# Performance work log

Hardware: AMD Instinct MI355X
Metric: run time of the kernel (lower is better)

Reference implementation:

```python
import jax, jax.numpy as jnp
import numpy as np

N, C, K, B, G = 32768, 128, 16, 4, 8
SCALE, BASE = 2.0, 10000.0

def _bn(x, gamma, beta, eps=1e-5):
    # torch BatchNorm1d (training): stats over all axes except channel (last)
    axes = tuple(range(x.ndim - 1))
    mean = x.mean(axes)
    var = x.var(axes)
    return (x - mean) / jnp.sqrt(var + eps) * gamma + beta

def _cayley_rope(x, coord, S_param):
    c = x.shape[-1]
    S = jnp.triu(S_param, 1)
    S = S - S.T
    I = jnp.eye(c, dtype=x.dtype)
    P = jnp.linalg.solve(I + S, I - S)  # (I+S)^-1 (I-S)
    xr = x @ P.T
    dpa = c // 3 // 2 * 2          # dim per axis (even)
    dr = dpa * 3                   # rotated dims
    inv_freq = 1.0 / (BASE ** (jnp.arange(0, dpa, 2, dtype=jnp.float32) / dpa))
    cs = coord * SCALE
    def rot(f, c1):
        ang = c1[:, None] * inv_freq[None, :]
        s, co = jnp.sin(ang), jnp.cos(ang)
        fr, fi = jnp.split(f, 2, axis=-1)
        return jnp.concatenate([fr * co - fi * s, fr * s + fi * co], -1)
    parts = [rot(xr[:, i * dpa:(i + 1) * dpa], cs[:, i]) for i in range(3)]
    out = jnp.concatenate(parts + [xr[:, dr:]], -1)
    return out @ P

def setup_inputs() -> dict:
    key = jax.random.key(0)
    ks = jax.random.split(key, 24)
    w = lambda k, i, o, s=0.02: jax.random.normal(k, (i, o), jnp.float32) * s
    inp = {
        'feat': jax.random.normal(ks[0], (N, C), jnp.float32),
        'coord': jax.random.uniform(ks[1], (N, 3), jnp.float32) * 10.0,
        'reference_index': jax.random.randint(ks[2], (N, K), 0, N),
        'offset': jnp.arange(1, B + 1, dtype=jnp.int32) * (N // B),
        'Wq': w(ks[3], C, C), 'bq': jnp.zeros((C,)),
        'gq': jnp.ones((C,)), 'bnq': jnp.zeros((C,)),
        'Wk': w(ks[4], C, C), 'bk': jnp.zeros((C,)),
        'gk': jnp.ones((C,)), 'bnk': jnp.zeros((C,)),
        'Wv': w(ks[5], C, C), 'bv': jnp.zeros((C,)),
        'S_param': jax.random.normal(ks[6], (C, C), jnp.float32) * 0.01,
        'Ww1': w(ks[7], C, G), 'bw1': jnp.zeros((G,)),
        'gw': jnp.ones((G,)), 'bnw': jnp.zeros((G,)),
        'Ww2': w(ks[8], G, G), 'bw2': jnp.zeros((G,)),
        'Wg1': w(ks[9], 2 * C, C), 'bg1': jnp.zeros((C,)),
        'gg': jnp.ones((C,)), 'bng': jnp.zeros((C,)),
        'Wg2': w(ks[10], C, G, 0.001), 'bg2': jnp.full((G,), 3.0),
    }
    return inp

def reference(feat, coord, reference_index, offset, Wq, bq, gq, bnq, Wk, bk, gk, bnk,
              Wv, bv, S_param, Ww1, bw1, gw, bnw, Ww2, bw2, Wg1, bg1, gg, bng, Wg2, bg2):
    q_raw = jax.nn.relu(_bn(feat @ Wq + bq, gq, bnq))
    k_raw = jax.nn.relu(_bn(feat @ Wk + bk, gk, bnk))
    value = feat @ Wv + bv
    q = _cayley_rope(q_raw, coord, S_param)
    k = _cayley_rope(k_raw, coord, S_param)
    kg = k[reference_index]            # [N,K,C] gather
    vg = value[reference_index]        # [N,K,C]
    rel = kg - q[:, None, :]
    geom = jax.nn.relu(_bn(rel @ Ww1 + bw1, gw, bnw)) @ Ww2 + bw2  # [N,K,G]
    seg = jnp.searchsorted(offset, jnp.arange(N), side='right')
    gmax = jax.ops.segment_max(q_raw, seg, num_segments=B)
    gate_in = jnp.concatenate([q_raw, gmax[seg]], -1)              # [N,2C]
    gate = jax.nn.sigmoid(jax.nn.relu(_bn(gate_in @ Wg1 + bg1, gg, bng)) @ Wg2 + bg2)  # [N,G]
    refined = geom * (1.0 + gate[:, None, :])
    attn = jax.nn.softmax(refined, axis=1)
    mask = jnp.sign(reference_index + 1).astype(attn.dtype)
    attn = attn * mask[:, :, None]
    vg4 = vg.reshape(N, K, G, C // G)
    out = jnp.einsum('nkgi,nkg->ngi', vg4, attn).reshape(N, C)
    return out
```

## Files before the change

### kernel.cpp

```cpp
#include <hip/hip_runtime.h>
#include <math.h>

#define N_PTS 32768
#define C_DIM 128
#define K_NB  16
#define G_DIM 8

#define OF_PW     0
#define OF_STATQ  1024
#define OF_STATK  1280
#define OF_STATG1 1536
#define OF_STATH  1792
#define OF_UMAXP  1808
#define OF_UMAXN  2320
#define OF_GSG    2832
#define OF_WQT    4096
#define OF_WKT    12288
#define OF_WVT    20480
#define OF_WG1T   28672
#define OF_PTMIT  36864
#define OF_QW     65536
#define OF_KW     327680
#define OF_GATE   589824
#define OF_G1     1048576
#define OF_V      5242880

typedef short bf16x8 __attribute__((ext_vector_type(8)));
typedef float f32x4  __attribute__((ext_vector_type(4)));

#define LSTR 136

__device__ __forceinline__ unsigned f2bf(float f) {
  unsigned u = __float_as_uint(f);
  return (u + 0x7fffu + ((u >> 16) & 1u)) >> 16;
}
__device__ __forceinline__ float bf2f(short s) {
  return __uint_as_float(((unsigned)(unsigned short)s) << 16);
}
__device__ __forceinline__ unsigned fenc(float f) {
  unsigned b = __float_as_uint(f);
  return (b & 0x80000000u) ? ~b : (b | 0x80000000u);
}
__device__ __forceinline__ float fdec(unsigned u) {
  unsigned b = (u & 0x80000000u) ? (u & 0x7fffffffu) : ~u;
  return __uint_as_float(b);
}
__device__ __forceinline__ bf16x8 pack_bf8(float4 a, float4 b) {
  bf16x8 r;
  r[0] = (short)f2bf(a.x); r[1] = (short)f2bf(a.y);
  r[2] = (short)f2bf(a.z); r[3] = (short)f2bf(a.w);
  r[4] = (short)f2bf(b.x); r[5] = (short)f2bf(b.y);
  r[6] = (short)f2bf(b.z); r[7] = (short)f2bf(b.w);
  return r;
}

__device__ __forceinline__ void g2l16(const void* g, void* l) {
  __builtin_amdgcn_global_load_lds(
      (const __attribute__((address_space(1))) void*)g,
      (__attribute__((address_space(3))) void*)l, 16, 0, 0);
}

__device__ __forceinline__ void stage_async(short* dst, const short* __restrict__ src, int tid) {
  int lane = tid & 63, wv = tid >> 6;
  #pragma unroll
  for (int it = 0; it < 8; ++it) {
    int chunk = it*256 + wv*64;
    int D = (chunk + lane)*16;
    int gs = D ^ (((D >> 8) & 7) << 4);
    g2l16((const char*)src + gs, (char*)dst + chunk*16);
  }
}

__device__ __forceinline__ f32x4 mfma1(const short* Bb, const bf16x8* a4, int row, int quad) {
  f32x4 ac = {0.f, 0.f, 0.f, 0.f};
  int sx = (row & 7) << 4;
  #pragma unroll
  for (int ks = 0; ks < 4; ++ks) {
    const char* p = (const char*)Bb + (((row*256) + ks*64 + quad*16) ^ sx);
    ac = __builtin_amdgcn_mfma_f32_16x16x32_bf16(a4[ks], *(const bf16x8*)p, ac, 0, 0, 0);
  }
  return ac;
}

__global__ __launch_bounds__(256) void cayley(const float* __restrict__ Sp,
    const float* __restrict__ Ww1,
    const float* __restrict__ Wq, const float* __restrict__ Wk,
    const float* __restrict__ Wv, const float* __restrict__ Wg1,
    short* __restrict__ WqT, short* __restrict__ WkT,
    short* __restrict__ WvT, short* __restrict__ Wg1T,
    short* __restrict__ PTmIT, float* __restrict__ PW,
    float* __restrict__ statz)
{
  __shared__ __align__(16) short Ssh[128*LSTR];
  __shared__ float x0[128], x1[128];
  int bx = blockIdx.x, tid = threadIdx.x;
  if (bx >= 64) {
    if (bx < 80) {
      int idx = bx - 64, widx = idx >> 2, qr = idx & 3;
      const float* src = (widx == 0) ? Wq : (widx == 1) ? Wk : (widx == 2) ? Wv : Wg1;
      short* dst = (widx == 0) ? WqT : (widx == 1) ? WkT : (widx == 2) ? WvT : Wg1T;
      const float4* s4 = (const float4*)src;
      short* T = Ssh;
      #pragma unroll
      for (int it = 0; it < 4; ++it) {
        int q = it*256 + tid; int kloc = q >> 5, n4 = q & 31;
        float4 v = s4[(qr*32 + kloc)*32 + n4];
        T[(n4*4+0)*40 + kloc] = (short)f2bf(v.x);
        T[(n4*4+1)*40 + kloc] = (short)f2bf(v.y);
        T[(n4*4+2)*40 + kloc] = (short)f2bf(v.z);
        T[(n4*4+3)*40 + kloc] = (short)f2bf(v.w);
      }
      __syncthreads();
      #pragma unroll
      for (int it = 0; it < 2; ++it) {
        int i2 = it*256 + tid;
        int n = i2 >> 2, part = i2 & 3;
        uint4 val = *(const uint4*)&T[n*40 + part*8];
        *(uint4*)&dst[n*128 + qr*32 + part*8] = val;
      }
    } else {
      #pragma unroll
      for (int it = 0; it < 8; ++it) {
        int idx = it*256 + tid;
        if (idx < 1808) statz[idx] = 0.f;
      }
    }
    return;
  }
  int c0 = bx*2, c1 = c0 + 1;
  {
    const float4* s4 = (const float4*)Sp;
    #pragma unroll
    for (int it = 0; it < 16; ++it) {
      int idx = it*256 + tid;
      int i = idx >> 5, j0 = (idx & 31) * 4;
      float4 v = s4[idx];
      #pragma unroll
      for (int u = 0; u < 4; ++u) {
        int j = j0 + u;
        float val = (&v.x)[u];
        if (j > i) {
          unsigned b = f2bf(val);
          Ssh[i*LSTR + j] = (short)b;
          Ssh[j*LSTR + i] = (short)(b ^ 0x8000u);
        } else if (j == i) {
          Ssh[i*LSTR + j] = 0;
        }
      }
    }
  }
  if (tid < 128) {
    x0[tid] = (tid == c0) ? 1.f : 0.f;
    x1[tid] = (tid == c1) ? 1.f : 0.f;
  }
  __syncthreads();
  int i = tid >> 1, h = tid & 1;
  const short* srow = &Ssh[i*LSTR + h*64];
  for (int t = 0; t < 16; ++t) {
    float a0 = 0.f, a1 = 0.f;
    #pragma unroll
    for (int jq = 0; jq < 16; ++jq) {
      short4 sv = *(const short4*)&srow[jq*4];
      #pragma unroll
      for (int u = 0; u < 4; ++u) {
        float s = bf2f((&sv.x)[u]);
        int j = h*64 + jq*4 + u;
        a0 = fmaf(s, x0[j], a0);
        a1 = fmaf(s, x1[j], a1);
      }
    }
    a0 += __shfl_xor(a0, 1);
    a1 += __shfl_xor(a1, 1);
    __syncthreads();
    if (h == 0) {
      x0[i] = a0 + ((i == c0) ? 1.f : 0.f);
      x1[i] = a1 + ((i == c1) ? 1.f : 0.f);
    }
    __syncthreads();
  }
  if (tid < 128) {
    PTmIT[c0*128 + tid] = (short)f2bf(2.f*x0[tid] - ((tid == c0) ? 2.f : 0.f));
  } else {
    int t = tid - 128;
    PTmIT[c1*128 + t] = (short)f2bf(2.f*x1[t] - ((t == c1) ? 2.f : 0.f));
  }
  if (tid < 16) {
    int cc = tid >> 3, g = tid & 7;
    const float* xv = cc ? x1 : x0;
    int c = cc ? c1 : c0;
    float acc = 0.f;
    #pragma unroll 8
    for (int j = 0; j < 128; ++j) acc = fmaf(xv[j], Ww1[j*8 + g], acc);
    PW[c*8 + g] = 2.f*acc - Ww1[c*8 + g];
  }
}

__global__ __launch_bounds__(256, 2) void qkv_mfma(const float* __restrict__ feat,
    const short* __restrict__ WqT, const short* __restrict__ WkT, const short* __restrict__ WvT,
    const float* __restrict__ bq, const float* __restrict__ bk, const float* __restrict__ bv,
    float* __restrict__ Vv,
    float* __restrict__ statq, float* __restrict__ statk,
    unsigned* __restrict__ umaxp, unsigned* __restrict__ umaxn)
{
  __shared__ __align__(16) short Bb0[128*128];
  __shared__ __align__(16) short Bb1[128*128];
  __shared__ float ssum[2][128], ssq[2][128];
  __shared__ unsigned ump[128], umn[128];
  int tid = threadIdx.x, row0 = blockIdx.x * 64, seg = row0 >> 13;
  int lane = tid & 63, w = tid >> 6, l15 = lane & 15, quad = lane >> 4;
  stage_async(Bb0, WqT, tid);
  if (tid < 128) {
    ssum[0][tid] = 0.f; ssum[1][tid] = 0.f;
    ssq[0][tid] = 0.f;  ssq[1][tid] = 0.f;
    ump[tid] = 0u; umn[tid] = 0u;
  }
  bf16x8 af[4];
  {
    long rbase = (long)(row0 + w*16 + l15) * 128;
    #pragma unroll
    for (int ks = 0; ks < 4; ++ks) {
      int c0 = ks*32 + quad*8;
      float4 v0 = *(const float4*)&feat[rbase + c0];
      float4 v1 = *(const float4*)&feat[rbase + c0 + 4];
      af[ks] = pack_bf8(v0, v1);
    }
  }
  __syncthreads();
  stage_async(Bb1, WkT, tid);
  {
    #pragma unroll
    for (int nt = 0; nt < 8; ++nt) {
      f32x4 ac = mfma1(Bb0, af, nt*16 + l15, quad);
      int col = nt*16 + l15;
      float bb = bq[col];
      float s = 0.f, s2 = 0.f, mx = -1e30f, mn = 1e30f;
      #pragma unroll
      for (int r = 0; r < 4; ++r) {
        float raw = ac[r];
        float v = raw + bb;
        s += v; s2 = fmaf(v, v, s2);
        mx = fmaxf(mx, raw); mn = fminf(mn, raw);
      }
      s += __shfl_xor(s, 16); s += __shfl_xor(s, 32);
      s2 += __shfl_xor(s2, 16); s2 += __shfl_xor(s2, 32);
      mx = fmaxf(mx, __shfl_xor(mx, 16)); mx = fmaxf(mx, __shfl_xor(mx, 32));
      mn = fminf(mn, __shfl_xor(mn, 16)); mn = fminf(mn, __shfl_xor(mn, 32));
      if (lane < 16) {
        atomicAdd(&ssum[0][col], s); atomicAdd(&ssq[0][col], s2);
        atomicMax(&ump[col], fenc(mx)); atomicMax(&umn[col], fenc(-mn));
      }
    }
  }
  __syncthreads();
  stage_async(Bb0, WvT, tid);
  {
    #pragma unroll
    for (int nt = 0; nt < 8; ++nt) {
      f32x4 ac = mfma1(Bb1, af, nt*16 + l15, quad);
      int col = nt*16 + l15;
      float bb = bk[col];
      float s = 0.f, s2 = 0.f;
      #pragma unroll
      for (int r = 0; r < 4; ++r) {
        float v = ac[r] + bb;
        s += v; s2 = fmaf(v, v, s2);
      }
      s += __shfl_xor(s, 16); s += __shfl_xor(s, 32);
      s2 += __shfl_xor(s2, 16); s2 += __shfl_xor(s2, 32);
      if (lane < 16) { atomicAdd(&ssum[1][col], s); atomicAdd(&ssq[1][col], s2); }
    }
  }
  __syncthreads();
  {
    #pragma unroll
    for (int nt = 0; nt < 8; ++nt) {
      f32x4 ac = mfma1(Bb0, af, nt*16 + l15, quad);
      int col = nt*16 + l15;
      float bb = bv[col];
      #pragma unroll
      for (int r = 0; r < 4; ++r)
        Vv[(long)(row0 + w*16 + quad*4 + r)*128 + col] = ac[r] + bb;
    }
  }
  __syncthreads();
  if (tid < 128) {
    atomicAdd(&statq[tid], ssum[0][tid]); atomicAdd(&statq[128 + tid], ssq[0][tid]);
    atomicAdd(&statk[tid], ssum[1][tid]); atomicAdd(&statk[128 + tid], ssq[1][tid]);
    atomicMax(&umaxp[seg*128 + tid], ump[tid]);
    atomicMax(&umaxn[seg*128 + tid], umn[tid]);
  }
}

__global__ __launch_bounds__(128) void gprep(
    const float* __restrict__ statq,
    const float* __restrict__ gq, const float* __restrict__ bnq,
    const float* __restrict__ bq,
    const unsigned* __restrict__ umaxp, const unsigned* __restrict__ umaxn,
    const float* __restrict__ Wg1, const float* __restrict__ bg1,
    float* __restrict__ gsgO)
{
  __shared__ float gml[128];
  int s = blockIdx.x, tid = threadIdx.x;
  const float invn = 1.f / 32768.f;
  {
    float m = statq[tid]*invn, vv = fmaf(-m, m, statq[128 + tid]*invn);
    float a = rsqrtf(vv + 1e-5f) * gq[tid];
    float b = fmaf(-m, a, bnq[tid]);
    float cb2 = fmaf(a, bq[tid], b);
    float mx = fdec(umaxp[s*128 + tid]);
    float mn = -fdec(umaxn[s*128 + tid]);
    gml[tid] = fmaxf(0.f, fmaxf(fmaf(a, mx, cb2), fmaf(a, mn, cb2)));
  }
  __syncthreads();
  float acc = bg1[tid];
  #pragma unroll 8
  for (int j = 0; j < 128; ++j)
    acc = fmaf(gml[j], Wg1[(128 + j)*128 + tid], acc);
  gsgO[s*128 + tid] = acc;
}

__global__ __launch_bounds__(256, 2) void rqkw(
    const float* __restrict__ feat,
    const short* __restrict__ WqT, const short* __restrict__ WkT,
    const short* __restrict__ PTmIT, const short* __restrict__ Wg1T,
    const float* __restrict__ coord,
    const float* __restrict__ bq, const float* __restrict__ bk,
    const float* __restrict__ statq, const float* __restrict__ statk,
    const float* __restrict__ gq, const float* __restrict__ bnq,
    const float* __restrict__ gk, const float* __restrict__ bnk,
    const float* __restrict__ gsgG,
    const float* __restrict__ PW, const float* __restrict__ bw1,
    float* __restrict__ qw, float* __restrict__ kw,
    float* __restrict__ g1, float* __restrict__ statg1)
{
  __shared__ __align__(16) char arena[81920];
  short* Bb0  = (short*)arena;
  short* Bb1  = (short*)(arena + 32768);
  char*  bnS  = arena + 65536;
  float* xsq  = (float*)arena;
  float* xsk  = (float*)(arena + 33792);
  float* pws  = (float*)(arena + 67584);
  float* ssum4 = (float*)(arena + 71680);
  float* ssq4  = (float*)(arena + 73728);
  int tid = threadIdx.x, row0 = blockIdx.x * 64, seg = row0 >> 13;
  int lane = tid & 63, w = tid >> 6, l15 = lane & 15, quad = lane >> 4;
  stage_async(Bb0, WqT, tid);
  stage_async(Bb1, WkT, tid);
  bf16x8 af[4];
  {
    long rbase = (long)(row0 + w*16 + l15) * 128;
    #pragma unroll
    for (int ks = 0; ks < 4; ++ks) {
      int c0 = ks*32 + quad*8;
      float4 v0 = *(const float4*)&feat[rbase + c0];
      float4 v1 = *(const float4*)&feat[rbase + c0 + 4];
      af[ks] = pack_bf8(v0, v1);
    }
  }
  float caRq[8], cbRq[8], caRk[8], cbRk[8];
  {
    const float invn = 1.f / 32768.f;
    #pragma unroll
    for (int nt = 0; nt < 8; ++nt) {
      int col = nt*16 + l15;
      float m = statq[col]*invn, vv = fmaf(-m, m, statq[128 + col]*invn);
      float a = rsqrtf(vv + 1e-5f) * gq[col];
      float b = fmaf(-m, a, bnq[col]);
      caRq[nt] = a; cbRq[nt] = fmaf(a, bq[col], b);
      m = statk[col]*invn; vv = fmaf(-m, m, statk[128 + col]*invn);
      a = rsqrtf(vv + 1e-5f) * gk[col];
      b = fmaf(-m, a, bnk[col]);
      caRk[nt] = a; cbRk[nt] = fmaf(a, bk[col], b);
    }
  }
  float gsR[8];
  #pragma unroll
  for (int nt = 0; nt < 8; ++nt)
    gsR[nt] = gsgG[seg*128 + nt*16 + l15];
  __syncthreads();
  float bnl_q[32], bnl_k[32];
  {
    #pragma unroll
    for (int nt = 0; nt < 8; ++nt) {
      f32x4 ac = mfma1(Bb0, af, nt*16 + l15, quad);
      int col = nt*16 + l15;
      float A = caRq[nt], B = cbRq[nt];
      #pragma unroll
      for (int r = 0; r < 4; ++r) {
        float v = fmaxf(0.f, fmaf(A, ac[r], B));
        bnl_q[nt*4 + r] = v;
        int row = w*16 + quad*4 + r;
        int ba = (row*256 + col*2) ^ ((row & 7) << 4);
        *(short*)(bnS + ba) = (short)f2bf(v);
      }
    }
  }
  __syncthreads();
  stage_async(Bb0, PTmIT, tid);
  {
    #pragma unroll
    for (int nt = 0; nt < 8; ++nt) {
      f32x4 ac = mfma1(Bb1, af, nt*16 + l15, quad);
      float A = caRk[nt], B = cbRk[nt];
      #pragma unroll
      for (int r = 0; r < 4; ++r)
        bnl_k[nt*4 + r] = fmaxf(0.f, fmaf(A, ac[r], B));
    }
  }
  __syncthreads();
  stage_async(Bb1, Wg1T, tid);
  bf16x8 af2q[4];
  {
    int rowA = w*16 + l15, sx2 = (rowA & 7) << 4;
    #pragma unroll
    for (int ks = 0; ks < 4; ++ks)
      af2q[ks] = *(const bf16x8*)(bnS + ((rowA*256 + ks*64 + quad*16) ^ sx2));
  }
  f32x4 accv_q[8];
  #pragma unroll
  for (int nt = 0; nt < 8; ++nt)
    accv_q[nt] = mfma1(Bb0, af2q, nt*16 + l15, quad);
  __syncthreads();
  {
    #pragma unroll
    for (int nt = 0; nt < 8; ++nt) {
      int col = nt*16 + l15;
      #pragma unroll
      for (int r = 0; r < 4; ++r) {
        int row = w*16 + quad*4 + r;
        int ba = (row*256 + col*2) ^ ((row & 7) << 4);
        *(short*)(bnS + ba) = (short)f2bf(bnl_k[nt*4 + r]);
      }
    }
  }
  __syncthreads();
  bf16x8 af2k[4];
  {
    int rowA = w*16 + l15, sx2 = (rowA & 7) << 4;
    #pragma unroll
    for (int ks = 0; ks < 4; ++ks)
      af2k[ks] = *(const bf16x8*)(bnS + ((rowA*256 + ks*64 + quad*16) ^ sx2));
  }
  f32x4 accv_k[8];
  float sred[8], s2red[8];
  {
    #pragma unroll
    for (int nt = 0; nt < 8; ++nt) {
      accv_k[nt] = mfma1(Bb0, af2k, nt*16 + l15, quad);
      f32x4 ac = mfma1(Bb1, af2q, nt*16 + l15, quad);
      int col = nt*16 + l15;
      float gsv = gsR[nt];
      float s = 0.f, s2 = 0.f;
      #pragma unroll
      for (int r = 0; r < 4; ++r) {
        float v = ac[r] + gsv;
        g1[(long)(row0 + w*16 + quad*4 + r)*128 + col] = v;
        s += v; s2 = fmaf(v, v, s2);
      }
      s += __shfl_xor(s, 16); s += __shfl_xor(s, 32);
      s2 += __shfl_xor(s2, 16); s2 += __shfl_xor(s2, 32);
      sred[nt] = s; s2red[nt] = s2;
    }
  }
  __syncthreads();
  {
    #pragma unroll
    for (int nt = 0; nt < 8; ++nt) {
      int col = nt*16 + l15;
      #pragma unroll
      for (int r = 0; r < 4; ++r) {
        int row = w*16 + quad*4 + r;
        xsq[row*132 + col] = accv_q[nt][r] + bnl_q[nt*4 + r];
        xsk[row*132 + col] = accv_k[nt][r] + bnl_k[nt*4 + r];
      }
    }
  }
  #pragma unroll
  for (int it = 0; it < 4; ++it) { int idx = tid + it*256; pws[idx] = PW[idx]; }
  if (lane < 16) {
    #pragma unroll
    for (int nt = 0; nt < 8; ++nt) {
      ssum4[w*128 + nt*16 + l15] = sred[nt];
      ssq4[w*128 + nt*16 + l15] = s2red[nt];
    }
  }
  __syncthreads();
  if (tid < 128) {
    float s = (ssum4[tid] + ssum4[128 + tid]) + (ssum4[256 + tid] + ssum4[384 + tid]);
    float s2 = (ssq4[tid] + ssq4[128 + tid]) + (ssq4[256 + tid] + ssq4[384 + tid]);
    atomicAdd(&statg1[tid], s);
    atomicAdd(&statg1[128 + tid], s2);
  }
  #pragma unroll
  for (int it = 0; it < 16; ++it) {
    int idx = it*256 + tid;
    int r = idx >> 6, s = idx & 63;
    if (s < 63) {
      int a3 = s / 21, j = s - a3*21;
      int cr = a3*42 + j;
      float invf = exp2f((float)(2*j) * (-13.287712379549449f / 42.f));
      float ang = coord[(row0 + r)*3 + a3] * (2.0f * invf);
      float sn, co; sincosf(ang, &sn, &co);
      float fr = xsq[r*132 + cr], fi = xsq[r*132 + cr + 21];
      xsq[r*132 + cr]      = fr*co - fi*sn;
      xsq[r*132 + cr + 21] = fr*sn + fi*co;
      fr = xsk[r*132 + cr]; fi = xsk[r*132 + cr + 21];
      xsk[r*132 + cr]      = fr*co - fi*sn;
      xsk[r*132 + cr + 21] = fr*sn + fi*co;
    }
  }
  __syncthreads();
  #pragma unroll
  for (int it = 0; it < 4; ++it) {
    int idx = it*256 + tid;
    int mat = idx >> 9, r2 = (idx >> 3) & 63, g = idx & 7;
    const float* x2 = mat ? xsk : xsq;
    float a0 = 0.f, a1 = 0.f, a2 = 0.f, a3 = 0.f;
    #pragma unroll 8
    for (int i = 0; i < 128; i += 4) {
      float4 xv = *(const float4*)&x2[r2*132 + i];
      a0 = fmaf(xv.x, pws[(i+0)*8 + g], a0);
      a1 = fmaf(xv.y, pws[(i+1)*8 + g], a1);
      a2 = fmaf(xv.z, pws[(i+2)*8 + g], a2);
      a3 = fmaf(xv.w, pws[(i+3)*8 + g], a3);
    }
    float acc = (a0 + a1) + (a2 + a3) + (mat ? bw1[g] : 0.f);
    float* dst = mat ? kw : qw;
    dst[(long)(row0 + r2)*8 + g] = acc;
  }
}

__global__ __launch_bounds__(256) void mid(
    const float* __restrict__ g1, const float* __restrict__ statg1,
    const float* __restrict__ ggm, const float* __restrict__ bng,
    const float* __restrict__ Wg2, const float* __restrict__ bg2,
    float* __restrict__ gate,
    const float* __restrict__ kw, const float* __restrict__ qw,
    const int* __restrict__ ref, float* __restrict__ stath)
{
  __shared__ float gs[32][132];
  __shared__ float w2s[128][8];
  __shared__ float cA[128], cB[128];
  __shared__ float red[256];
  int tid = threadIdx.x;
  if (blockIdx.x < 1024) {
    int row0 = blockIdx.x * 32;
    #pragma unroll
    for (int it = 0; it < 4; ++it) { int idx = tid + it*256; w2s[idx >> 3][idx & 7] = Wg2[idx]; }
    if (tid < 128) {
      const float invn = 1.f / 32768.f;
      float m = statg1[tid]*invn, v = fmaf(-m, m, statg1[128 + tid]*invn);
      float a = rsqrtf(v + 1e-5f) * ggm[tid];
      cA[tid] = a; cB[tid] = fmaf(-m, a, bng[tid]);
    }
    #pragma unroll
    for (int it = 0; it < 4; ++it) {
      int idx = tid + it*256; int r = idx >> 5, cq = idx & 31;
      *(float4*)&gs[r][cq*4] = *(const float4*)&g1[(long)(row0 + r)*128 + cq*4];
    }
    __syncthreads();
    int r = tid >> 3, g = tid & 7;
    float acc = bg2[g];
    #pragma unroll 8
    for (int c2 = 0; c2 < 128; ++c2) {
      float act = fmaxf(0.f, fmaf(gs[r][c2], cA[c2], cB[c2]));
      acc = fmaf(act, w2s[c2][g], acc);
    }
    gate[(long)(row0 + r)*8 + g] = 1.f / (1.f + expf(-acc));
  } else {
    long base = (long)(blockIdx.x - 1024) * 4096;
    float s = 0.f, sq = 0.f;
    for (int it = 0; it < 16; ++it) {
      long idx = base + it*256 + tid;
      int n = (int)(idx >> 7); int kk = (int)((idx >> 3) & 15); int g = (int)(idx & 7);
      int r = ref[n*16 + kk];
      float h = kw[(long)r*8 + g] - qw[(long)n*8 + g];
      s += h; sq = fmaf(h, h, sq);
    }
    red[tid] = s; __syncthreads();
    for (int d = 128; d >= 8; d >>= 1) { if (tid < d) red[tid] += red[tid + d]; __syncthreads(); }
    if (tid < 8) atomicAdd(&stath[tid], red[tid]);
    __syncthreads();
    red[tid] = sq; __syncthreads();
    for (int d = 128; d >= 8; d >>= 1) { if (tid < d) red[tid] += red[tid + d]; __syncthreads(); }
    if (tid < 8) atomicAdd(&stath[8 + tid], red[tid]);
  }
}

__global__ __launch_bounds__(256) void attn_out(const float* __restrict__ qw, const float* __restrict__ kw,
                                                const float* __restrict__ stath,
                                                const float* __restrict__ gw, const float* __restrict__ bnw,
                                                const float* __restrict__ Ww2, const float* __restrict__ bw2,
                                                const float* __restrict__ gate, const int* __restrict__ ref,
                                                const float* __restrict__ v, float* __restrict__ out)
{
  __shared__ float sm1[2][16][9];
  __shared__ float sm2[2][16][9];
  __shared__ int   smr[2][16];
  int tid = threadIdx.x; int rh = tid >> 7, t = tid & 127;
  int n = blockIdx.x * 2 + rh;
  int kk = t >> 3, g = t & 7;
  if (t < 16) smr[rh][t] = ref[n*16 + t];
  __syncthreads();
  const float invnk = 1.f / 524288.f;
  float m0 = stath[g]*invnk, v0 = fmaf(-m0, m0, stath[8 + g]*invnk);
  float aw = rsqrtf(v0 + 1e-5f) * gw[g];
  float bw = fmaf(-m0, aw, bnw[g]);
  int rr = smr[rh][kk];
  float h = kw[(long)rr*8 + g] - qw[(long)n*8 + g];
  sm1[rh][kk][g] = fmaxf(0.f, fmaf(h, aw, bw));
  __syncthreads();
  float acc = bw2[g];
  #pragma unroll
  for (int g2 = 0; g2 < 8; ++g2) acc = fmaf(sm1[rh][kk][g2], Ww2[g2*8 + g], acc);
  float refined = acc * (1.f + gate[(long)n*8 + g]);
  sm2[rh][kk][g] = refined;
  __syncthreads();
  float mx = -1e30f;
  #pragma unroll
  for (int k2 = 0; k2 < 16; ++k2) mx = fmaxf(mx, sm2[rh][k2][g]);
  float e = expf(refined - mx);
  sm1[rh][kk][g] = e;
  __syncthreads();
  float ssum = 0.f;
  #pragma unroll
  for (int k2 = 0; k2 < 16; ++k2) ssum += sm1[rh][k2][g];
  float mask = ((rr + 1) > 0) ? 1.f : (((rr + 1) == 0) ? 0.f : -1.f);
  float attn = e / ssum * mask;
  sm2[rh][kk][g] = attn;
  __syncthreads();
  float o = 0.f;
  #pragma unroll
  for (int k2 = 0; k2 < 16; ++k2) {
    o = fmaf(v[(long)smr[rh][k2]*128 + t], sm2[rh][k2][t >> 4], o);
  }
  out[(long)n*128 + t] = o;
}

extern "C" void kernel_launch(void* const* d_in, const int* in_sizes, int n_in,
                              void* d_out, int out_size, void* d_ws, size_t ws_size,
                              hipStream_t stream)
{
  const float* feat  = (const float*)d_in[0];
  const float* coord = (const float*)d_in[1];
  const int*   ref   = (const int*)d_in[2];
  const float* Wq  = (const float*)d_in[4];
  const float* bq  = (const float*)d_in[5];
  const float* gq  = (const float*)d_in[6];
  const float* bnq = (const float*)d_in[7];
  const float* Wk  = (const float*)d_in[8];
  const float* bk  = (const float*)d_in[9];
  const float* gk  = (const float*)d_in[10];
  const float* bnk = (const float*)d_in[11];
  const float* Wv  = (const float*)d_in[12];
  const float* bv  = (const float*)d_in[13];
  const float* Sp  = (const float*)d_in[14];
  const float* Ww1 = (const float*)d_in[15];
  const float* bw1 = (const float*)d_in[16];
  const float* gw  = (const float*)d_in[17];
  const float* bnw = (const float*)d_in[18];
  const float* Ww2 = (const float*)d_in[19];
  const float* bw2 = (const float*)d_in[20];
  const float* Wg1 = (const float*)d_in[21];
  const float* bg1 = (const float*)d_in[22];
  const float* ggm = (const float*)d_in[23];
  const float* bng = (const float*)d_in[24];
  const float* Wg2 = (const float*)d_in[25];
  const float* bg2 = (const float*)d_in[26];
  float* out = (float*)d_out;

  float* W = (float*)d_ws;
  float* PW = W + OF_PW;
  short* WqT   = (short*)(W + OF_WQT);
  short* WkT   = (short*)(W + OF_WKT);
  short* WvT   = (short*)(W + OF_WVT);
  short* Wg1T  = (short*)(W + OF_WG1T);
  short* PTmIT = (short*)(W + OF_PTMIT);
  float* G1 = W + OF_G1;
  float* Vv = W + OF_V;

  cayley<<<81, 256, 0, stream>>>(Sp, Ww1, Wq, Wk, Wv, Wg1,
                                 WqT, WkT, WvT, Wg1T, PTmIT, PW, W + OF_STATQ);
  qkv_mfma<<<512, 256, 0, stream>>>(feat, WqT, WkT, WvT, bq, bk, bv, Vv,
                                    W + OF_STATQ, W + OF_STATK,
                                    (unsigned*)(W + OF_UMAXP), (unsigned*)(W + OF_UMAXN));
  gprep<<<4, 128, 0, stream>>>(W + OF_STATQ, gq, bnq, bq,
                               (const unsigned*)(W + OF_UMAXP),
                               (const unsigned*)(W + OF_UMAXN),
                               Wg1, bg1, W + OF_GSG);
  rqkw<<<512, 256, 0, stream>>>(feat, WqT, WkT, PTmIT, Wg1T, coord,
                                bq, bk,
                                W + OF_STATQ, W + OF_STATK,
                                gq, bnq, gk, bnk,
                                W + OF_GSG, PW, bw1,
                                W + OF_QW, W + OF_KW, G1, W + OF_STATG1);
  mid<<<2048, 256, 0, stream>>>(G1, W + OF_STATG1, ggm, bng, Wg2, bg2, W + OF_GATE,
                                W + OF_KW, W + OF_QW, ref, W + OF_STATH);
  attn_out<<<16384, 256, 0, stream>>>(W + OF_QW, W + OF_KW, W + OF_STATH, gw, bnw, Ww2, bw2,
                                      W + OF_GATE, ref, Vv, out);
}
```

Baseline: 290.1 us.

## Fuse gate computation into attention kernel and split h-statistics kernel

```diff
diff --git a/kernel.cpp b/kernel.cpp
--- a/kernel.cpp
+++ b/kernel.cpp
@@ -530,35 +530,65 @@
   }
 }
 
-__global__ __launch_bounds__(256) void mid(
+__global__ __launch_bounds__(256) void hstat_k(
+    const float* __restrict__ kw, const float* __restrict__ qw,
+    const int* __restrict__ ref, float* __restrict__ stath)
+{
+  __shared__ float red[256];
+  int tid = threadIdx.x;
+  long base = (long)blockIdx.x * 4096;
+  float s = 0.f, sq = 0.f;
+  for (int it = 0; it < 16; ++it) {
+    long idx = base + it*256 + tid;
+    int n = (int)(idx >> 7); int kk = (int)((idx >> 3) & 15); int g = (int)(idx & 7);
+    int r = ref[n*16 + kk];
+    float h = kw[(long)r*8 + g] - qw[(long)n*8 + g];
+    s += h; sq = fmaf(h, h, sq);
+  }
+  red[tid] = s; __syncthreads();
+  for (int d = 128; d >= 8; d >>= 1) { if (tid < d) red[tid] += red[tid + d]; __syncthreads(); }
+  if (tid < 8) atomicAdd(&stath[tid], red[tid]);
+  __syncthreads();
+  red[tid] = sq; __syncthreads();
+  for (int d = 128; d >= 8; d >>= 1) { if (tid < d) red[tid] += red[tid + d]; __syncthreads(); }
+  if (tid < 8) atomicAdd(&stath[8 + tid], red[tid]);
+}
+
+__global__ __launch_bounds__(256) void attn2(
     const float* __restrict__ g1, const float* __restrict__ statg1,
     const float* __restrict__ ggm, const float* __restrict__ bng,
     const float* __restrict__ Wg2, const float* __restrict__ bg2,
-    float* __restrict__ gate,
-    const float* __restrict__ kw, const float* __restrict__ qw,
-    const int* __restrict__ ref, float* __restrict__ stath)
+    const float* __restrict__ qw, const float* __restrict__ kw,
+    const float* __restrict__ stath,
+    const float* __restrict__ gw, const float* __restrict__ bnw,
+    const float* __restrict__ Ww2, const float* __restrict__ bw2,
+    const int* __restrict__ ref, const float* __restrict__ v,
+    float* __restrict__ out)
 {
   __shared__ float gs[32][132];
   __shared__ float w2s[128][8];
   __shared__ float cA[128], cB[128];
-  __shared__ float red[256];
+  __shared__ float gt[32][8];
+  __shared__ float sm1[2][16][9];
+  __shared__ float sm2[2][16][9];
+  __shared__ int   smr[2][16];
   int tid = threadIdx.x;
-  if (blockIdx.x < 1024) {
-    int row0 = blockIdx.x * 32;
-    #pragma unroll
-    for (int it = 0; it < 4; ++it) { int idx = tid + it*256; w2s[idx >> 3][idx & 7] = Wg2[idx]; }
-    if (tid < 128) {
-      const float invn = 1.f / 32768.f;
-      float m = statg1[tid]*invn, v = fmaf(-m, m, statg1[128 + tid]*invn);
-      float a = rsqrtf(v + 1e-5f) * ggm[tid];
-      cA[tid] = a; cB[tid] = fmaf(-m, a, bng[tid]);
-    }
-    #pragma unroll
-    for (int it = 0; it < 4; ++it) {
-      int idx = tid + it*256; int r = idx >> 5, cq = idx & 31;
-      *(float4*)&gs[r][cq*4] = *(const float4*)&g1[(long)(row0 + r)*128 + cq*4];
-    }
-    __syncthreads();
+  int row0 = blockIdx.x * 32;
+  #pragma unroll
+  for (int it = 0; it < 4; ++it) { int idx = tid + it*256; w2s[idx >> 3][idx & 7] = Wg2[idx]; }
+  if (tid < 128) {
+    const float invn = 1.f / 32768.f;
+    float m = statg1[tid]*invn, vv = fmaf(-m, m, statg1[128 + tid]*invn);
+    float a = rsqrtf(vv + 1e-5f) * ggm[tid];
+    cA[tid] = a; cB[tid] = fmaf(-m, a, bng[tid]);
+  }
+  #pragma unroll
+  for (int it = 0; it < 4; ++it) {
+    int idx = tid + it*256; int r = idx >> 5, cq = idx & 31;
+    *(float4*)&gs[r][cq*4] = *(const float4*)&g1[(long)(row0 + r)*128 + cq*4];
+  }
+  __syncthreads();
+  {
     int r = tid >> 3, g = tid & 7;
     float acc = bg2[g];
     #pragma unroll 8
@@ -566,75 +596,55 @@
       float act = fmaxf(0.f, fmaf(gs[r][c2], cA[c2], cB[c2]));
       acc = fmaf(act, w2s[c2][g], acc);
     }
-    gate[(long)(row0 + r)*8 + g] = 1.f / (1.f + expf(-acc));
-  } else {
-    long base = (long)(blockIdx.x - 1024) * 4096;
-    float s = 0.f, sq = 0.f;
-    for (int it = 0; it < 16; ++it) {
-      long idx = base + it*256 + tid;
-      int n = (int)(idx >> 7); int kk = (int)((idx >> 3) & 15); int g = (int)(idx & 7);
-      int r = ref[n*16 + kk];
-      float h = kw[(long)r*8 + g] - qw[(long)n*8 + g];
-      s += h; sq = fmaf(h, h, sq);
-    }
-    red[tid] = s; __syncthreads();
-    for (int d = 128; d >= 8; d >>= 1) { if (tid < d) red[tid] += red[tid + d]; __syncthreads(); }
-    if (tid < 8) atomicAdd(&stath[tid], red[tid]);
-    __syncthreads();
-    red[tid] = sq; __syncthreads();
-    for (int d = 128; d >= 8; d >>= 1) { if (tid < d) red[tid] += red[tid + d]; __syncthreads(); }
-    if (tid < 8) atomicAdd(&stath[8 + tid], red[tid]);
-  }
-}
-
-__global__ __launch_bounds__(256) void attn_out(const float* __restrict__ qw, const float* __restrict__ kw,
-                                                const float* __restrict__ stath,
-                                                const float* __restrict__ gw, const float* __restrict__ bnw,
-                                                const float* __restrict__ Ww2, const float* __restrict__ bw2,
-                                                const float* __restrict__ gate, const int* __restrict__ ref,
-                                                const float* __restrict__ v, float* __restrict__ out)
-{
-  __shared__ float sm1[2][16][9];
-  __shared__ float sm2[2][16][9];
-  __shared__ int   smr[2][16];
-  int tid = threadIdx.x; int rh = tid >> 7, t = tid & 127;
-  int n = blockIdx.x * 2 + rh;
+    gt[r][g] = 1.f / (1.f + expf(-acc));
+  }
+  int rh = tid >> 7, t = tid & 127;
   int kk = t >> 3, g = t & 7;
-  if (t < 16) smr[rh][t] = ref[n*16 + t];
-  __syncthreads();
   const float invnk = 1.f / 524288.f;
   float m0 = stath[g]*invnk, v0 = fmaf(-m0, m0, stath[8 + g]*invnk);
   float aw = rsqrtf(v0 + 1e-5f) * gw[g];
   float bw = fmaf(-m0, aw, bnw[g]);
-  int rr = smr[rh][kk];
-  float h = kw[(long)rr*8 + g] - qw[(long)n*8 + g];
-  sm1[rh][kk][g] = fmaxf(0.f, fmaf(h, aw, bw));
-  __syncthreads();
-  float acc = bw2[g];
-  #pragma unroll
-  for (int g2 = 0; g2 < 8; ++g2) acc = fmaf(sm1[rh][kk][g2], Ww2[g2*8 + g], acc);
-  float refined = acc * (1.f + gate[(long)n*8 + g]);
-  sm2[rh][kk][g] = refined;
-  __syncthreads();
-  float mx = -1e30f;
-  #pragma unroll
-  for (int k2 = 0; k2 < 16; ++k2) mx = fmaxf(mx, sm2[rh][k2][g]);
-  float e = expf(refined - mx);
-  sm1[rh][kk][g] = e;
-  __syncthreads();
-  float ssum = 0.f;
-  #pragma unroll
-  for (int k2 = 0; k2 < 16; ++k2) ssum += sm1[rh][k2][g];
-  float mask = ((rr + 1) > 0) ? 1.f : (((rr + 1) == 0) ? 0.f : -1.f);
-  float attn = e / ssum * mask;
-  sm2[rh][kk][g] = attn;
-  __syncthreads();
-  float o = 0.f;
-  #pragma unroll
-  for (int k2 = 0; k2 < 16; ++k2) {
-    o = fmaf(v[(long)smr[rh][k2]*128 + t], sm2[rh][k2][t >> 4], o);
-  }
-  out[(long)n*128 + t] = o;
+  float w2r[8];
+  #pragma unroll
+  for (int g2 = 0; g2 < 8; ++g2) w2r[g2] = Ww2[g2*8 + g];
+  float bw2g = bw2[g];
+  __syncthreads();
+  for (int itr = 0; itr < 16; ++itr) {
+    int nl = itr*2 + rh;
+    int n = row0 + nl;
+    if (t < 16) smr[rh][t] = ref[n*16 + t];
+    __syncthreads();
+    int rr = smr[rh][kk];
+    float h = kw[(long)rr*8 + g] - qw[(long)n*8 + g];
+    sm1[rh][kk][g] = fmaxf(0.f, fmaf(h, aw, bw));
+    __syncthreads();
+    float acc = bw2g;
+    #pragma unroll
+    for (int g2 = 0; g2 < 8; ++g2) acc = fmaf(sm1[rh][kk][g2], w2r[g2], acc);
+    float refined = acc * (1.f + gt[nl][g]);
+    sm2[rh][kk][g] = refined;
+    __syncthreads();
+    float mx = -1e30f;
+    #pragma unroll
+    for (int k2 = 0; k2 < 16; ++k2) mx = fmaxf(mx, sm2[rh][k2][g]);
+    float e = expf(refined - mx);
+    sm1[rh][kk][g] = e;
+    __syncthreads();
+    float ssum = 0.f;
+    #pragma unroll
+    for (int k2 = 0; k2 < 16; ++k2) ssum += sm1[rh][k2][g];
+    float mask = ((rr + 1) > 0) ? 1.f : (((rr + 1) == 0) ? 0.f : -1.f);
+    float attn = e / ssum * mask;
+    sm2[rh][kk][g] = attn;
+    __syncthreads();
+    float o = 0.f;
+    #pragma unroll
+    for (int k2 = 0; k2 < 16; ++k2) {
+      o = fmaf(v[(long)smr[rh][k2]*128 + t], sm2[rh][k2][t >> 4], o);
+    }
+    out[(long)n*128 + t] = o;
+    __syncthreads();
+  }
 }
 
 extern "C" void kernel_launch(void* const* d_in, const int* in_sizes, int n_in,
@@ -694,8 +704,8 @@
                                 gq, bnq, gk, bnk,
                                 W + OF_GSG, PW, bw1,
                                 W + OF_QW, W + OF_KW, G1, W + OF_STATG1);
-  mid<<<2048, 256, 0, stream>>>(G1, W + OF_STATG1, ggm, bng, Wg2, bg2, W + OF_GATE,
-                                W + OF_KW, W + OF_QW, ref, W + OF_STATH);
-  attn_out<<<16384, 256, 0, stream>>>(W + OF_QW, W + OF_KW, W + OF_STATH, gw, bnw, Ww2, bw2,
-                                      W + OF_GATE, ref, Vv, out);
-}
+  hstat_k<<<1024, 256, 0, stream>>>(W + OF_KW, W + OF_QW, ref, W + OF_STATH);
+  attn2<<<1024, 256, 0, stream>>>(G1, W + OF_STATG1, ggm, bng, Wg2, bg2,
+                                  W + OF_QW, W + OF_KW, W + OF_STATH,
+                                  gw, bnw, Ww2, bw2, ref, Vv, out);
+}
```

Result: slower. 296.0 us (+2.0%).
